# Optimization experiments

Hardware: AMD Instinct MI355X
Metric: run time of the kernel (lower is better)

The kernel has to match this reference:

```python
import jax, jax.numpy as jnp
import numpy as np

N, E, F_IN, H, D, K = 50000, 800000, 128, 128, 64, 4

def setup_inputs():
    key = jax.random.key(0)
    ks = jax.random.split(key, 10)
    def rnd(k, shape, s=0.05):
        return jax.random.normal(k, shape, dtype=jnp.float32) * s
    return {
        "x": jax.random.normal(ks[0], (N, F_IN), dtype=jnp.float32),
        "edge_index": jax.random.randint(ks[1], (2, E), 0, N, dtype=jnp.int32),
        "W1": rnd(ks[2], (F_IN, H)),
        "b1": jnp.zeros((H,), jnp.float32),
        "a1": jnp.full((), 0.25, jnp.float32),
        "W2": rnd(ks[3], (H, H)),
        "b2": jnp.zeros((H,), jnp.float32),
        "a2": jnp.full((), 0.25, jnp.float32),
        "Wmu": rnd(ks[4], (K, H, D)),
        "bmu": jnp.zeros((K, D), jnp.float32),
        "amu": jnp.full((K,), 0.25, jnp.float32),
        "Wlv": rnd(ks[5], (K, H, D)),
        "blv": jnp.zeros((K, D), jnp.float32),
        "alv": jnp.full((K,), 0.25, jnp.float32),
        "Wr": rnd(ks[6], (K, D)),
        "br": jnp.zeros((K,), jnp.float32),
        "eps": jax.random.normal(ks[7], (N, K * D), dtype=jnp.float32),
    }

def _prelu(v, a):
    return jnp.where(v >= 0, v, a * v)

def _gcn_norm(edge_index):
    # PyG GCNConv defaults: add self-loops, symmetric deg^{-1/2} normalization
    loop = jnp.arange(N, dtype=edge_index.dtype)
    src = jnp.concatenate([edge_index[0], loop])
    dst = jnp.concatenate([edge_index[1], loop])
    deg = jax.ops.segment_sum(jnp.ones_like(dst, jnp.float32), dst, num_segments=N)
    dinv = jnp.where(deg > 0, jax.lax.rsqrt(deg), 0.0)
    norm = dinv[src] * dinv[dst]  # per-edge coefficient
    return src, dst, norm

def reference(x, edge_index, W1, b1, a1, W2, b2, a2, Wmu, bmu, amu, Wlv, blv, alv, Wr, br, eps):
    src, dst, norm = _gcn_norm(edge_index)
    def prop(h):  # gather -> normalize -> scatter-add
        return jax.ops.segment_sum(h[src] * norm[:, None], dst, num_segments=N)
    # shared GCN stack: GCNConv = propagate(x @ W) + b, then PReLU
    h = _prelu(prop(x @ W1) + b1, a1)
    hgcn = _prelu(prop(h @ W2) + b2, a2)
    # per-branch GCNConvs share the input; propagation is linear, so
    # propagate(hgcn @ Wk) == propagate(hgcn) @ Wk -> propagate once for all K
    p = prop(hgcn)  # (N, H)
    mu_k = _prelu(jnp.einsum('nh,khd->knd', p, Wmu) + bmu[:, None, :], amu[:, None, None])  # (K,N,D)
    lv_k = jax.nn.sigmoid(_prelu(jnp.einsum('nh,khd->knd', p, Wlv) + blv[:, None, :], alv[:, None, None]))
    mu = jnp.transpose(mu_k, (1, 0, 2)).reshape(N, K * D)
    logvar = jnp.transpose(lv_k, (1, 0, 2)).reshape(N, K * D)
    hk = eps * jnp.exp(0.5 * logvar) + mu  # reparameterize
    r = jax.nn.sigmoid(jnp.einsum('nkd,kd->nk', hk.reshape(N, K, D), Wr) + br)  # (N,K)
    return hgcn, logvar, mu, hk, r
```

## Files before the change

kernel.cpp:

```cpp
#include <hip/hip_runtime.h>
#include <math.h>

#define N_NODES 50000
#define N_EDGES 800000
#define HDIM 128
#define KD 256

typedef float f32x4 __attribute__((ext_vector_type(4)));
typedef short s16x8 __attribute__((ext_vector_type(8)));

__device__ __forceinline__ ushort f2b(float f) {
    union { float f; unsigned u; } x; x.f = f;
    unsigned u = x.u;
    return (ushort)((u + 0x7FFF + ((u >> 16) & 1)) >> 16);
}
__device__ __forceinline__ float b2f(ushort h) {
    union { unsigned u; float f; } x; x.u = ((unsigned)h) << 16; return x.f;
}

__global__ void zero_int(int* __restrict__ p, int n) {
    int i = blockIdx.x * blockDim.x + threadIdx.x;
    if (i < n) p[i] = 0;
}

__global__ void count_deg(const int* __restrict__ dst, int* __restrict__ cnt, int e) {
    int i = blockIdx.x * blockDim.x + threadIdx.x;
    if (i < e) atomicAdd(&cnt[dst[i]], 1);
}

__global__ void calc_dinv(const int* __restrict__ cnt, float* __restrict__ dinv, int n) {
    int i = blockIdx.x * blockDim.x + threadIdx.x;
    if (i < n) dinv[i] = rsqrtf((float)(cnt[i] + 1));
}

__global__ __launch_bounds__(1024)
void scan_kernel(const int* __restrict__ cnt, int* __restrict__ offsets,
                 int* __restrict__ cursor, int n) {
    __shared__ int wsum[16];
    __shared__ int carry_s;
    int tid = threadIdx.x;
    int lane = tid & 63, wid = tid >> 6;
    if (tid == 0) carry_s = 0;
    __syncthreads();
    for (int base = 0; base < n; base += 1024) {
        int i = base + tid;
        int v = (i < n) ? cnt[i] : 0;
        int x = v;
        #pragma unroll
        for (int off = 1; off < 64; off <<= 1) {
            int t = __shfl_up(x, off, 64);
            if (lane >= off) x += t;
        }
        if (lane == 63) wsum[wid] = x;
        __syncthreads();
        if (wid == 0) {
            int w = (lane < 16) ? wsum[lane] : 0;
            #pragma unroll
            for (int off = 1; off < 16; off <<= 1) {
                int t = __shfl_up(w, off, 64);
                if (lane >= off) w += t;
            }
            if (lane < 16) wsum[lane] = w;
        }
        __syncthreads();
        int waveoff = (wid > 0) ? wsum[wid - 1] : 0;
        int incl = x + waveoff;
        int carry = carry_s;
        int excl = carry + incl - v;
        if (i < n) { offsets[i] = excl; cursor[i] = excl; }
        __syncthreads();
        if (tid == 1023) carry_s = carry + incl;
        __syncthreads();
    }
    if (tid == 0) offsets[n] = carry_s;
}

__global__ void fill_csr(const int* __restrict__ src, const int* __restrict__ dst,
                         int* __restrict__ cursor, int* __restrict__ csr, int e) {
    int i = blockIdx.x * blockDim.x + threadIdx.x;
    if (i < e) {
        int d = dst[i];
        int pos = atomicAdd(&cursor[d], 1);
        csr[pos] = src[i];
    }
}

__global__ void conv_x(const float4* __restrict__ x, ushort4* __restrict__ o,
                       const float* __restrict__ dinv, int n4) {
    int i = blockIdx.x * 256 + threadIdx.x;
    if (i >= n4) return;
    int row = i >> 5;
    float dv = dinv[row];
    float4 v = x[i];
    ushort4 u;
    u.x = f2b(v.x * dv); u.y = f2b(v.y * dv);
    u.z = f2b(v.z * dv); u.w = f2b(v.w * dv);
    o[i] = u;
}

__global__ void prep_w(const float* __restrict__ W1, const float* __restrict__ W2,
                       const float* __restrict__ Wmu, const float* __restrict__ Wlv,
                       ushort* __restrict__ w1t, ushort* __restrict__ w2t,
                       ushort* __restrict__ bt3) {
    int i = blockIdx.x * 256 + threadIdx.x;
    if (i < 16384) {
        int nn = i >> 7, k = i & 127;
        w1t[i] = f2b(W1[k * 128 + nn]);
    } else if (i < 32768) {
        int j = i - 16384; int nn = j >> 7, k = j & 127;
        w2t[j] = f2b(W2[k * 128 + nn]);
    } else if (i < 98304) {
        int j = i - 32768;
        int h = j & 127; int nk = j >> 7; int nn = nk & 127; int k = nk >> 7;
        float v = (nn < 64) ? Wmu[k * 8192 + h * 64 + nn]
                            : Wlv[k * 8192 + h * 64 + (nn - 64)];
        bt3[j] = f2b(v);
    }
}

__global__ __launch_bounds__(256)
void prop_b(const ushort2* __restrict__ hin, ushort2* __restrict__ hout,
            const int* __restrict__ csr, const int* __restrict__ offsets,
            const float* __restrict__ dinv, int n) {
    int gw = blockIdx.x * 4 + (threadIdx.x >> 6);
    int lane = threadIdx.x & 63;
    if (gw >= n) return;
    int beg = offsets[gw], end = offsets[gw + 1];
    float ax = 0.f, ay = 0.f;
    for (int i = beg; i < end; i += 64) {
        int cnt = end - i; if (cnt > 64) cnt = 64;
        int sidx = (lane < cnt) ? csr[i + lane] : 0;
        int j = 0;
        for (; j + 1 < cnt; j += 2) {
            int s0 = __shfl(sidx, j, 64);
            int s1 = __shfl(sidx, j + 1, 64);
            ushort2 v0 = hin[(size_t)s0 * 64 + lane];
            ushort2 v1 = hin[(size_t)s1 * 64 + lane];
            ax += b2f(v0.x) + b2f(v1.x);
            ay += b2f(v0.y) + b2f(v1.y);
        }
        if (j < cnt) {
            int s0 = __shfl(sidx, j, 64);
            ushort2 v0 = hin[(size_t)s0 * 64 + lane];
            ax += b2f(v0.x);
            ay += b2f(v0.y);
        }
    }
    ushort2 sv = hin[(size_t)gw * 64 + lane];
    ax += b2f(sv.x); ay += b2f(sv.y);
    float dn = dinv[gw];
    ax *= dn; ay *= dn;
    ushort2 o; o.x = f2b(ax); o.y = f2b(ay);
    hout[(size_t)gw * 64 + lane] = o;
}

template<int MODE>
__global__ __launch_bounds__(256)
void gemm12(const ushort* __restrict__ A, const ushort* __restrict__ Bt,
            const float* __restrict__ bias, const float* __restrict__ alpha,
            const float* __restrict__ dinv,
            float* __restrict__ Cf, ushort* __restrict__ Cb, int nrows) {
    __shared__ char As[32768];
    __shared__ char Bs[32768];
    int tid = threadIdx.x;
    int row0 = blockIdx.x * 128;
    #pragma unroll
    for (int it = 0; it < 8; ++it) {
        int idx = tid + it * 256;
        int r = idx >> 4, cb = (idx & 15) << 4;
        int sw = cb ^ ((r & 15) << 4);
        uint4 v = make_uint4(0, 0, 0, 0);
        int row = row0 + r;
        if (row < nrows) v = *(const uint4*)((const char*)A + (size_t)row * 256 + cb);
        *(uint4*)(As + r * 256 + sw) = v;
        uint4 bv = *(const uint4*)((const char*)Bt + (size_t)idx * 16);
        *(uint4*)(Bs + r * 256 + sw) = bv;
    }
    __syncthreads();

    int w = tid >> 6, lane = tid & 63;
    int bq = lane >> 4, tr = lane & 15;
    f32x4 acc[2][8];
    #pragma unroll
    for (int mi = 0; mi < 2; ++mi)
        #pragma unroll
        for (int nj = 0; nj < 8; ++nj)
            acc[mi][nj] = (f32x4){0.f, 0.f, 0.f, 0.f};

    #pragma unroll
    for (int s = 0; s < 4; ++s) {
        int xoff = (s * 64 + bq * 16) ^ ((tr & 15) << 4);
        s16x8 af[2], bfr[8];
        #pragma unroll
        for (int mi = 0; mi < 2; ++mi)
            af[mi] = *(const s16x8*)(As + (w * 32 + mi * 16 + tr) * 256 + xoff);
        #pragma unroll
        for (int nj = 0; nj < 8; ++nj)
            bfr[nj] = *(const s16x8*)(Bs + (nj * 16 + tr) * 256 + xoff);
        #pragma unroll
        for (int mi = 0; mi < 2; ++mi)
            #pragma unroll
            for (int nj = 0; nj < 8; ++nj)
                acc[mi][nj] = __builtin_amdgcn_mfma_f32_16x16x32_bf16(af[mi], bfr[nj], acc[mi][nj], 0, 0, 0);
    }

    int g = lane >> 4, c = lane & 15;
    float aval = alpha[0];
    float bb[8];
    #pragma unroll
    for (int nj = 0; nj < 8; ++nj) bb[nj] = bias[nj * 16 + c];
    #pragma unroll
    for (int mi = 0; mi < 2; ++mi) {
        #pragma unroll
        for (int j = 0; j < 4; ++j) {
            int row = row0 + w * 32 + mi * 16 + g * 4 + j;
            if (row >= nrows) continue;
            float dv = dinv[row];
            #pragma unroll
            for (int nj = 0; nj < 8; ++nj) {
                int col = nj * 16 + c;
                float t = acc[mi][nj][j] + bb[nj];
                t = t >= 0.f ? t : aval * t;
                if (MODE) Cf[(size_t)row * 128 + col] = t;
                Cb[(size_t)row * 128 + col] = f2b(t * dv);
            }
        }
    }
}

template<int FUSED>
__global__ __launch_bounds__(256)
void gemm3(const ushort* __restrict__ A, const ushort* __restrict__ Bt3,
           const float* __restrict__ bmu, const float* __restrict__ blv,
           const float* __restrict__ amu, const float* __restrict__ alv,
           const float* __restrict__ Wr, const float* __restrict__ br,
           const float* __restrict__ eps,
           float* __restrict__ out_mu, float* __restrict__ out_lv,
           float* __restrict__ out_hk, float* __restrict__ out_r, int nrows) {
    __shared__ char As[32768];
    __shared__ char Bs[32768];
    int tid = threadIdx.x;
    int k = blockIdx.x;
    int row0 = blockIdx.y * 128;
    const ushort* Bt = Bt3 + (size_t)k * 16384;
    #pragma unroll
    for (int it = 0; it < 8; ++it) {
        int idx = tid + it * 256;
        int r = idx >> 4, cb = (idx & 15) << 4;
        int sw = cb ^ ((r & 15) << 4);
        uint4 v = make_uint4(0, 0, 0, 0);
        int row = row0 + r;
        if (row < nrows) v = *(const uint4*)((const char*)A + (size_t)row * 256 + cb);
        *(uint4*)(As + r * 256 + sw) = v;
        uint4 bv = *(const uint4*)((const char*)Bt + (size_t)idx * 16);
        *(uint4*)(Bs + r * 256 + sw) = bv;
    }
    __syncthreads();

    int w = tid >> 6, lane = tid & 63;
    int bq = lane >> 4, tr = lane & 15;
    f32x4 acc[2][8];
    #pragma unroll
    for (int mi = 0; mi < 2; ++mi)
        #pragma unroll
        for (int nj = 0; nj < 8; ++nj)
            acc[mi][nj] = (f32x4){0.f, 0.f, 0.f, 0.f};

    #pragma unroll
    for (int s = 0; s < 4; ++s) {
        int xoff = (s * 64 + bq * 16) ^ ((tr & 15) << 4);
        s16x8 af[2], bfr[8];
        #pragma unroll
        for (int mi = 0; mi < 2; ++mi)
            af[mi] = *(const s16x8*)(As + (w * 32 + mi * 16 + tr) * 256 + xoff);
        #pragma unroll
        for (int nj = 0; nj < 8; ++nj)
            bfr[nj] = *(const s16x8*)(Bs + (nj * 16 + tr) * 256 + xoff);
        #pragma unroll
        for (int mi = 0; mi < 2; ++mi)
            #pragma unroll
            for (int nj = 0; nj < 8; ++nj)
                acc[mi][nj] = __builtin_amdgcn_mfma_f32_16x16x32_bf16(af[mi], bfr[nj], acc[mi][nj], 0, 0, 0);
    }

    int g = lane >> 4, c = lane & 15;
    float amuv = amu[k], alvv = alv[k];
    float brk = br[k];
    float bmv[4], blvb[4], wrv[4];
    #pragma unroll
    for (int nj = 0; nj < 4; ++nj) {
        int d = nj * 16 + c;
        bmv[nj] = bmu[k * 64 + d];
        blvb[nj] = blv[k * 64 + d];
        wrv[nj] = FUSED ? Wr[k * 64 + d] : 0.f;
    }
    #pragma unroll
    for (int mi = 0; mi < 2; ++mi) {
        float rsum[4] = {0.f, 0.f, 0.f, 0.f};
        #pragma unroll
        for (int j = 0; j < 4; ++j) {
            int row = row0 + w * 32 + mi * 16 + g * 4 + j;
            if (row >= nrows) continue;
            #pragma unroll
            for (int nj = 0; nj < 4; ++nj) {
                int d = nj * 16 + c;
                size_t oc = (size_t)row * KD + k * 64 + d;
                float m_ = acc[mi][nj][j] + bmv[nj];
                m_ = m_ >= 0.f ? m_ : amuv * m_;
                float l_ = acc[mi][nj + 4][j] + blvb[nj];
                l_ = l_ >= 0.f ? l_ : alvv * l_;
                l_ = 1.f / (1.f + __expf(-l_));
                out_mu[oc] = m_;
                out_lv[oc] = l_;
                if (FUSED) {
                    float h = fmaf(eps[oc], __expf(0.5f * l_), m_);
                    out_hk[oc] = h;
                    rsum[j] = fmaf(h, wrv[nj], rsum[j]);
                }
            }
        }
        if (FUSED) {
            #pragma unroll
            for (int j = 0; j < 4; ++j) {
                float t = rsum[j];
                t += __shfl_xor(t, 1, 64);
                t += __shfl_xor(t, 2, 64);
                t += __shfl_xor(t, 4, 64);
                t += __shfl_xor(t, 8, 64);
                if (c == 0) {
                    int row = row0 + w * 32 + mi * 16 + g * 4 + j;
                    if (row < nrows)
                        out_r[(size_t)row * 4 + k] = 1.f / (1.f + __expf(-(t + brk)));
                }
            }
        }
    }
}

__global__ void hk_kernel(const float* __restrict__ mu, const float* __restrict__ lv,
                          const float* __restrict__ eps, const float* __restrict__ Wr,
                          const float* __restrict__ br, float* __restrict__ hk,
                          float* __restrict__ r, int n) {
    int gw = (blockIdx.x * blockDim.x + threadIdx.x) >> 6;
    int lane = threadIdx.x & 63;
    if (gw >= n) return;
    size_t base = (size_t)gw * KD;
    #pragma unroll
    for (int k = 0; k < 4; ++k) {
        int c = k * 64 + lane;
        float m = mu[base + c], v = lv[base + c], e = eps[base + c];
        float h = fmaf(e, __expf(0.5f * v), m);
        hk[base + c] = h;
        float t = h * Wr[k * 64 + lane];
        #pragma unroll
        for (int off = 32; off >= 1; off >>= 1) t += __shfl_xor(t, off, 64);
        if (lane == 0) r[(size_t)gw * 4 + k] = 1.f / (1.f + __expf(-(t + br[k])));
    }
}

extern "C" void kernel_launch(void* const* d_in, const int* in_sizes, int n_in,
                              void* d_out, int out_size, void* d_ws, size_t ws_size,
                              hipStream_t stream) {
    const float* x   = (const float*)d_in[0];
    const int*   ei  = (const int*)d_in[1];
    const float* W1  = (const float*)d_in[2];
    const float* b1  = (const float*)d_in[3];
    const float* a1  = (const float*)d_in[4];
    const float* W2  = (const float*)d_in[5];
    const float* b2  = (const float*)d_in[6];
    const float* a2  = (const float*)d_in[7];
    const float* Wmu = (const float*)d_in[8];
    const float* bmu = (const float*)d_in[9];
    const float* amu = (const float*)d_in[10];
    const float* Wlv = (const float*)d_in[11];
    const float* blv = (const float*)d_in[12];
    const float* alv = (const float*)d_in[13];
    const float* Wr  = (const float*)d_in[14];
    const float* br  = (const float*)d_in[15];
    const float* eps = (const float*)d_in[16];

    float* out      = (float*)d_out;
    float* out_hgcn = out;
    float* out_lv   = out + (size_t)N_NODES * HDIM;
    float* out_mu   = out_lv + (size_t)N_NODES * KD;
    float* out_hk   = out_mu + (size_t)N_NODES * KD;
    float* out_r    = out_hk + (size_t)N_NODES * KD;

    char* ws = (char*)d_ws;
    int*    cnt     = (int*)ws;
    int*    offsets = (int*)(ws + 204800);
    int*    cursor  = (int*)(ws + 409600);
    int*    csr     = (int*)(ws + 614400);
    float*  dinv    = (float*)(ws + 3814400);
    ushort* w1t     = (ushort*)(ws + 4014592);
    ushort* w2t     = (ushort*)(ws + 4047360);
    ushort* bt3     = (ushort*)(ws + 4080128);

    ushort* S0 = (ushort*)out_hk;
    ushort* S1 = S0 + (size_t)N_NODES * HDIM;
    ushort* S2 = S1 + (size_t)N_NODES * HDIM;
    ushort* S3 = S2 + (size_t)N_NODES * HDIM;

    const size_t P_OFF = 4211264;
    const bool fused = ws_size >= P_OFF + (size_t)N_NODES * HDIM * 2;
    ushort* P = fused ? (ushort*)(ws + P_OFF) : S1;

    const int* e_src = ei;
    const int* e_dst = ei + N_EDGES;

    zero_int <<<(N_NODES + 255) / 256, 256, 0, stream>>>(cnt, N_NODES);
    count_deg<<<(N_EDGES + 255) / 256, 256, 0, stream>>>(e_dst, cnt, N_EDGES);
    calc_dinv<<<(N_NODES + 255) / 256, 256, 0, stream>>>(cnt, dinv, N_NODES);
    scan_kernel<<<1, 1024, 0, stream>>>(cnt, offsets, cursor, N_NODES);
    fill_csr <<<(N_EDGES + 255) / 256, 256, 0, stream>>>(e_src, e_dst, cursor, csr, N_EDGES);

    prep_w<<<384, 256, 0, stream>>>(W1, W2, Wmu, Wlv, w1t, w2t, bt3);
    conv_x<<<(N_NODES * 32 + 255) / 256, 256, 0, stream>>>((const float4*)x, (ushort4*)S0, dinv, N_NODES * 32);

    prop_b<<<12500, 256, 0, stream>>>((const ushort2*)S0, (ushort2*)S1, csr, offsets, dinv, N_NODES);
    gemm12<0><<<391, 256, 0, stream>>>(S1, w1t, b1, a1, dinv, nullptr, S2, N_NODES);
    prop_b<<<12500, 256, 0, stream>>>((const ushort2*)S2, (ushort2*)S3, csr, offsets, dinv, N_NODES);
    gemm12<1><<<391, 256, 0, stream>>>(S3, w2t, b2, a2, dinv, out_hgcn, S0, N_NODES);
    prop_b<<<12500, 256, 0, stream>>>((const ushort2*)S0, (ushort2*)P, csr, offsets, dinv, N_NODES);

    dim3 g3(4, 391);
    if (fused) {
        gemm3<1><<<g3, 256, 0, stream>>>(P, bt3, bmu, blv, amu, alv, Wr, br, eps,
                                         out_mu, out_lv, out_hk, out_r, N_NODES);
    } else {
        gemm3<0><<<g3, 256, 0, stream>>>(P, bt3, bmu, blv, amu, alv, Wr, br, eps,
                                         out_mu, out_lv, out_hk, out_r, N_NODES);
        hk_kernel<<<12500, 256, 0, stream>>>(out_mu, out_lv, eps, Wr, br, out_hk, out_r, N_NODES);
    }
}
```

Measured before the change: 357.5 us.

## Parallelize degree prefix scan and widen gather loads in propagation

Replaces the single-block serial prefix scan over 50k node degrees with a three-kernel multi-block scan (block-local scan, top-level scan of block sums, add-back). Rewrites the propagation kernel so each wave splits into four 16-lane groups. Each lane loads 8 bf16 values (16 bytes) per neighbor, and the group partials are combined with cross-lane shuffles at the end. The intent is to remove a long single-workgroup serial stage and to raise memory-level parallelism in the gathers. The cost is two extra kernel launches and an extra reduction step per node.

```diff
diff --git a/kernel.cpp b/kernel.cpp
--- a/kernel.cpp
+++ b/kernel.cpp
@@ -34,45 +34,59 @@
 }
 
 __global__ __launch_bounds__(1024)
-void scan_kernel(const int* __restrict__ cnt, int* __restrict__ offsets,
-                 int* __restrict__ cursor, int n) {
+void scan_blk(const int* __restrict__ cnt, int* __restrict__ offsets,
+              int* __restrict__ blocksum, int n) {
     __shared__ int wsum[16];
-    __shared__ int carry_s;
     int tid = threadIdx.x;
+    int i = blockIdx.x * 1024 + tid;
     int lane = tid & 63, wid = tid >> 6;
-    if (tid == 0) carry_s = 0;
+    int v = (i < n) ? cnt[i] : 0;
+    int x = v;
+    #pragma unroll
+    for (int off = 1; off < 64; off <<= 1) {
+        int t = __shfl_up(x, off, 64);
+        if (lane >= off) x += t;
+    }
+    if (lane == 63) wsum[wid] = x;
     __syncthreads();
-    for (int base = 0; base < n; base += 1024) {
-        int i = base + tid;
-        int v = (i < n) ? cnt[i] : 0;
-        int x = v;
-        #pragma unroll
-        for (int off = 1; off < 64; off <<= 1) {
-            int t = __shfl_up(x, off, 64);
-            if (lane >= off) x += t;
-        }
-        if (lane == 63) wsum[wid] = x;
-        __syncthreads();
-        if (wid == 0) {
-            int w = (lane < 16) ? wsum[lane] : 0;
-            #pragma unroll
-            for (int off = 1; off < 16; off <<= 1) {
-                int t = __shfl_up(w, off, 64);
-                if (lane >= off) w += t;
-            }
-            if (lane < 16) wsum[lane] = w;
-        }
-        __syncthreads();
-        int waveoff = (wid > 0) ? wsum[wid - 1] : 0;
-        int incl = x + waveoff;
-        int carry = carry_s;
-        int excl = carry + incl - v;
-        if (i < n) { offsets[i] = excl; cursor[i] = excl; }
-        __syncthreads();
-        if (tid == 1023) carry_s = carry + incl;
-        __syncthreads();
-    }
-    if (tid == 0) offsets[n] = carry_s;
+    if (wid == 0) {
+        int w = (lane < 16) ? wsum[lane] : 0;
+        #pragma unroll
+        for (int off = 1; off < 16; off <<= 1) {
+            int t = __shfl_up(w, off, 64);
+            if (lane >= off) w += t;
+        }
+        if (lane < 16) wsum[lane] = w;
+    }
+    __syncthreads();
+    int waveoff = (wid > 0) ? wsum[wid - 1] : 0;
+    if (i < n) offsets[i] = x + waveoff - v;
+    if (tid == 1023) blocksum[blockIdx.x] = x + waveoff;
+}
+
+__global__ void scan_top(const int* __restrict__ blocksum, int* __restrict__ blockpref,
+                         int* __restrict__ offsets, int nb, int n) {
+    int lane = threadIdx.x;
+    int v = (lane < nb) ? blocksum[lane] : 0;
+    int x = v;
+    #pragma unroll
+    for (int off = 1; off < 64; off <<= 1) {
+        int t = __shfl_up(x, off, 64);
+        if (lane >= off) x += t;
+    }
+    if (lane < nb) blockpref[lane] = x - v;
+    if (lane == 63) offsets[n] = x;
+}
+
+__global__ __launch_bounds__(1024)
+void scan_add(int* __restrict__ offsets, int* __restrict__ cursor,
+              const int* __restrict__ blockpref, int n) {
+    int i = blockIdx.x * 1024 + threadIdx.x;
+    if (i < n) {
+        int o = offsets[i] + blockpref[blockIdx.x];
+        offsets[i] = o;
+        cursor[i] = o;
+    }
 }
 
 __global__ void fill_csr(const int* __restrict__ src, const int* __restrict__ dst,
@@ -119,39 +133,57 @@
 }
 
 __global__ __launch_bounds__(256)
-void prop_b(const ushort2* __restrict__ hin, ushort2* __restrict__ hout,
+void prop_b(const ushort* __restrict__ hin, ushort* __restrict__ hout,
             const int* __restrict__ csr, const int* __restrict__ offsets,
             const float* __restrict__ dinv, int n) {
     int gw = blockIdx.x * 4 + (threadIdx.x >> 6);
+    if (gw >= n) return;
     int lane = threadIdx.x & 63;
-    if (gw >= n) return;
+    int grp = lane >> 4, gl = lane & 15;
+    int coff = gl << 3;
     int beg = offsets[gw], end = offsets[gw + 1];
-    float ax = 0.f, ay = 0.f;
-    for (int i = beg; i < end; i += 64) {
-        int cnt = end - i; if (cnt > 64) cnt = 64;
-        int sidx = (lane < cnt) ? csr[i + lane] : 0;
-        int j = 0;
-        for (; j + 1 < cnt; j += 2) {
+    float a0[8] = {0.f,0.f,0.f,0.f,0.f,0.f,0.f,0.f};
+    float a1[8] = {0.f,0.f,0.f,0.f,0.f,0.f,0.f,0.f};
+    for (int base = beg; base < end; base += 64) {
+        int cnt = end - base; if (cnt > 64) cnt = 64;
+        int sidx = (lane < cnt) ? csr[base + lane] : 0;
+        int j = grp;
+        for (; j + 4 < cnt; j += 8) {
             int s0 = __shfl(sidx, j, 64);
-            int s1 = __shfl(sidx, j + 1, 64);
-            ushort2 v0 = hin[(size_t)s0 * 64 + lane];
-            ushort2 v1 = hin[(size_t)s1 * 64 + lane];
-            ax += b2f(v0.x) + b2f(v1.x);
-            ay += b2f(v0.y) + b2f(v1.y);
+            int s1 = __shfl(sidx, j + 4, 64);
+            s16x8 v0 = *(const s16x8*)(hin + (s0 << 7) + coff);
+            s16x8 v1 = *(const s16x8*)(hin + (s1 << 7) + coff);
+            #pragma unroll
+            for (int q = 0; q < 8; ++q) {
+                a0[q] += b2f((ushort)v0[q]);
+                a1[q] += b2f((ushort)v1[q]);
+            }
         }
         if (j < cnt) {
             int s0 = __shfl(sidx, j, 64);
-            ushort2 v0 = hin[(size_t)s0 * 64 + lane];
-            ax += b2f(v0.x);
-            ay += b2f(v0.y);
-        }
-    }
-    ushort2 sv = hin[(size_t)gw * 64 + lane];
-    ax += b2f(sv.x); ay += b2f(sv.y);
-    float dn = dinv[gw];
-    ax *= dn; ay *= dn;
-    ushort2 o; o.x = f2b(ax); o.y = f2b(ay);
-    hout[(size_t)gw * 64 + lane] = o;
+            s16x8 v0 = *(const s16x8*)(hin + (s0 << 7) + coff);
+            #pragma unroll
+            for (int q = 0; q < 8; ++q) a0[q] += b2f((ushort)v0[q]);
+        }
+    }
+    #pragma unroll
+    for (int q = 0; q < 8; ++q) {
+        float t = a0[q] + a1[q];
+        t += __shfl_xor(t, 16, 64);
+        t += __shfl_xor(t, 32, 64);
+        a0[q] = t;
+    }
+    if (grp == 0) {
+        s16x8 sv = *(const s16x8*)(hin + (gw << 7) + coff);
+        float dn = dinv[gw];
+        s16x8 o;
+        #pragma unroll
+        for (int q = 0; q < 8; ++q) {
+            float t = (a0[q] + b2f((ushort)sv[q])) * dn;
+            o[q] = (short)f2b(t);
+        }
+        *(s16x8*)(hout + (gw << 7) + coff) = o;
+    }
 }
 
 template<int MODE>
@@ -387,41 +419,46 @@
     float* out_r    = out_hk + (size_t)N_NODES * KD;
 
     char* ws = (char*)d_ws;
-    int*    cnt     = (int*)ws;
-    int*    offsets = (int*)(ws + 204800);
-    int*    cursor  = (int*)(ws + 409600);
-    int*    csr     = (int*)(ws + 614400);
-    float*  dinv    = (float*)(ws + 3814400);
-    ushort* w1t     = (ushort*)(ws + 4014592);
-    ushort* w2t     = (ushort*)(ws + 4047360);
-    ushort* bt3     = (ushort*)(ws + 4080128);
+    int*    cnt      = (int*)ws;
+    int*    offsets  = (int*)(ws + 204800);
+    int*    cursor   = (int*)(ws + 409600);
+    int*    csr      = (int*)(ws + 614400);
+    float*  dinv     = (float*)(ws + 3814400);
+    ushort* w1t      = (ushort*)(ws + 4014592);
+    ushort* w2t      = (ushort*)(ws + 4047360);
+    ushort* bt3      = (ushort*)(ws + 4080128);
+    int*    blocksum = (int*)(ws + 4211200);
+    int*    blockpref= (int*)(ws + 4211456);
 
     ushort* S0 = (ushort*)out_hk;
     ushort* S1 = S0 + (size_t)N_NODES * HDIM;
     ushort* S2 = S1 + (size_t)N_NODES * HDIM;
     ushort* S3 = S2 + (size_t)N_NODES * HDIM;
 
-    const size_t P_OFF = 4211264;
+    const size_t P_OFF = 4211712;
     const bool fused = ws_size >= P_OFF + (size_t)N_NODES * HDIM * 2;
     ushort* P = fused ? (ushort*)(ws + P_OFF) : S1;
 
     const int* e_src = ei;
     const int* e_dst = ei + N_EDGES;
+    const int NB = (N_NODES + 1023) / 1024;
 
     zero_int <<<(N_NODES + 255) / 256, 256, 0, stream>>>(cnt, N_NODES);
     count_deg<<<(N_EDGES + 255) / 256, 256, 0, stream>>>(e_dst, cnt, N_EDGES);
     calc_dinv<<<(N_NODES + 255) / 256, 256, 0, stream>>>(cnt, dinv, N_NODES);
-    scan_kernel<<<1, 1024, 0, stream>>>(cnt, offsets, cursor, N_NODES);
+    scan_blk <<<NB, 1024, 0, stream>>>(cnt, offsets, blocksum, N_NODES);
+    scan_top <<<1, 64, 0, stream>>>(blocksum, blockpref, offsets, NB, N_NODES);
+    scan_add <<<NB, 1024, 0, stream>>>(offsets, cursor, blockpref, N_NODES);
     fill_csr <<<(N_EDGES + 255) / 256, 256, 0, stream>>>(e_src, e_dst, cursor, csr, N_EDGES);
 
     prep_w<<<384, 256, 0, stream>>>(W1, W2, Wmu, Wlv, w1t, w2t, bt3);
     conv_x<<<(N_NODES * 32 + 255) / 256, 256, 0, stream>>>((const float4*)x, (ushort4*)S0, dinv, N_NODES * 32);
 
-    prop_b<<<12500, 256, 0, stream>>>((const ushort2*)S0, (ushort2*)S1, csr, offsets, dinv, N_NODES);
+    prop_b<<<12500, 256, 0, stream>>>(S0, S1, csr, offsets, dinv, N_NODES);
     gemm12<0><<<391, 256, 0, stream>>>(S1, w1t, b1, a1, dinv, nullptr, S2, N_NODES);
-    prop_b<<<12500, 256, 0, stream>>>((const ushort2*)S2, (ushort2*)S3, csr, offsets, dinv, N_NODES);
+    prop_b<<<12500, 256, 0, stream>>>(S2, S3, csr, offsets, dinv, N_NODES);
     gemm12<1><<<391, 256, 0, stream>>>(S3, w2t, b2, a2, dinv, out_hgcn, S0, N_NODES);
-    prop_b<<<12500, 256, 0, stream>>>((const ushort2*)S0, (ushort2*)P, csr, offsets, dinv, N_NODES);
+    prop_b<<<12500, 256, 0, stream>>>(S0, P, csr, offsets, dinv, N_NODES);
 
     dim3 g3(4, 391);
     if (fused) {
```

Result: faster. 291.7 us (-18.4%).
